# Kernel tuning notes

Hardware: AMD Instinct MI355X
Metric: run time of the kernel (lower is better)

## Reference

```python
import jax, jax.numpy as jnp
import numpy as np

B, S, D, H, DFF = 4, 1024, 1024, 16, 4096
DK = D // H
EPS = 1e-6


def setup_inputs() -> dict:
    key = jax.random.key(0)
    ks = jax.random.split(key, 16)
    sd = 0.02
    inp = {
        "x_v": jax.random.normal(ks[0], (B, S, D), jnp.float32),
        "x_k": jax.random.normal(ks[1], (B, S, D), jnp.float32),
        "x_q": jax.random.normal(ks[2], (B, S, D), jnp.float32),
        "mask": jnp.zeros((B, 1, S), jnp.float32),
        # per-head projections stacked: [H, D, DK]
        "wq": jax.random.normal(ks[3], (H, D, DK), jnp.float32) * sd,
        "bq": jnp.zeros((H, DK), jnp.float32),
        "wk": jax.random.normal(ks[4], (H, D, DK), jnp.float32) * sd,
        "bk": jnp.zeros((H, DK), jnp.float32),
        "wv": jax.random.normal(ks[5], (H, D, DK), jnp.float32) * sd,
        "bv": jnp.zeros((H, DK), jnp.float32),
        "w0": jax.random.normal(ks[6], (D, D), jnp.float32) * sd,
        "b0": jnp.zeros((D,), jnp.float32),
        "ln1_g": jnp.ones((D,), jnp.float32),
        "ln1_b": jnp.zeros((D,), jnp.float32),
        "ff1_w": jax.random.normal(ks[7], (D, DFF), jnp.float32) * sd,
        "ff1_b": jnp.zeros((DFF,), jnp.float32),
        "ff2_w": jax.random.normal(ks[8], (DFF, D), jnp.float32) * sd,
        "ff2_b": jnp.zeros((D,), jnp.float32),
        "ln2_g": jnp.ones((D,), jnp.float32),
        "ln2_b": jnp.zeros((D,), jnp.float32),
    }
    return inp


def layer_norm(x, g, b):
    mu = jnp.mean(x, axis=-1, keepdims=True)
    var = jnp.mean(jnp.square(x - mu), axis=-1, keepdims=True)
    return (x - mu) * jax.lax.rsqrt(var + EPS) * g + b


def reference(x_v, x_k, x_q, mask, wq, bq, wk, bk, wv, bv, w0, b0,
              ln1_g, ln1_b, ff1_w, ff1_b, ff2_w, ff2_b, ln2_g, ln2_b):
    # --- Multi-head attention (heads batched instead of Python loop) ---
    q = jnp.einsum('bsd,hdk->bhsk', x_q, wq) + bq[:, None, :]  # [B,H,S,DK]
    k = jnp.einsum('bsd,hdk->bhsk', x_k, wk) + bk[:, None, :]
    v = jnp.einsum('bsd,hdk->bhsk', x_v, wv) + bv[:, None, :]
    scores = jnp.einsum('bhqk,bhsk->bhqs', q, k) / jnp.sqrt(jnp.float32(DK))
    scores = scores + mask[:, None, :, :] * (-1e9)  # mask broadcast over heads
    attn_w = jax.nn.softmax(scores, axis=-1)        # [B,H,S,S]
    attn = jnp.einsum('bhqs,bhsk->bhqk', attn_w, v)  # [B,H,S,DK]
    concat = attn.transpose(0, 2, 1, 3).reshape(B, S, D)
    mha_out = concat @ w0 + b0
    # --- Residual + LayerNorm 1 (dropout is identity at inference) ---
    sub1 = layer_norm(x_q + mha_out, ln1_g, ln1_b)
    # --- Point-wise FFN ---
    ffn = jax.nn.relu(sub1 @ ff1_w + ff1_b) @ ff2_w + ff2_b
    # --- Residual + LayerNorm 2 ---
    out = layer_norm(sub1 + ffn, ln2_g, ln2_b)
    # original returns the attention weights of the LAST head only
    return out, attn_w[:, -1]
```

## Files before the change

kernel.cpp:

```cpp
#include <hip/hip_runtime.h>
#include <hip/hip_bf16.h>
#include <stdint.h>

#define DEV __device__ __forceinline__

typedef uint16_t u16;
typedef __attribute__((ext_vector_type(8))) short s16x8;
typedef __attribute__((ext_vector_type(8))) unsigned short u16x8;
typedef __attribute__((ext_vector_type(4))) unsigned short u16x4;
typedef __attribute__((ext_vector_type(4))) float f32x4;

constexpr int CB = 4;
constexpr int CS = 1024;
constexpr int CD = 1024;
constexpr int CH = 16;
constexpr int CDFF = 4096;
constexpr int LSTR = 72;

DEV float b2f(u16 u) { union { uint32_t i; float f; } v; v.i = (uint32_t)u << 16; return v.f; }
DEV u16 f2b(float f) {
  union { float f; uint32_t i; } v; v.f = f;
  uint32_t r = v.i + 0x7fffu + ((v.i >> 16) & 1u);
  return (u16)(r >> 16);
}

using as1v = const __attribute__((address_space(1))) void;
using as3v = __attribute__((address_space(3))) void;
DEV void g2l16(const u16* g, u16* l) {
  __builtin_amdgcn_global_load_lds((as1v*)g, (as3v*)l, 16, 0, 0);
}

__global__ void detect_dtype(const uint32_t* __restrict__ w, uint32_t* __restrict__ flag) {
  if (threadIdx.x == 0 && blockIdx.x == 0) {
    flag[0] = (w[0] == 0x3F800000u) ? 1u : 0u;
    flag[1] = 0u;
  }
}

__global__ __launch_bounds__(256)
void cvt3(const void* __restrict__ s0, const void* __restrict__ s1, const void* __restrict__ s2,
          u16* __restrict__ d0, u16* __restrict__ d1, u16* __restrict__ d2,
          const uint32_t* __restrict__ flag)
{
  const void* s = blockIdx.z == 0 ? s0 : (blockIdx.z == 1 ? s1 : s2);
  u16* d        = blockIdx.z == 0 ? d0 : (blockIdx.z == 1 ? d1 : d2);
  size_t i = ((size_t)blockIdx.x * 256 + threadIdx.x) * 4;
  if (flag[0]) {
    const float* f = (const float*)s;
    u16x4 o;
#pragma unroll
    for (int j = 0; j < 4; j++) o[j] = f2b(f[i + j]);
    *(u16x4*)(d + i) = o;
  } else {
    *(u16x4*)(d + i) = *(const u16x4*)((const u16*)s + i);
  }
}

struct SmallCvt {
  const void* src[11];
  u16* dst[11];
  int n[11];
};
__global__ __launch_bounds__(256)
void cvt_small(SmallCvt sc, const uint32_t* __restrict__ flag)
{
  int idx = blockIdx.x * 256 + threadIdx.x;
#pragma unroll
  for (int a = 0; a < 11; a++) {
    if (idx < sc.n[a]) {
      if (flag[0]) sc.dst[a][idx] = f2b(((const float*)sc.src[a])[idx]);
      else         sc.dst[a][idx] = ((const u16*)sc.src[a])[idx];
      return;
    }
    idx -= sc.n[a];
  }
}

__global__ __launch_bounds__(256)
void transpose64d(const void* __restrict__ in, u16* __restrict__ out,
                  int in_rs, long long in_ys, long long in_zs,
                  int out_rs, long long out_ys, long long out_zs,
                  const uint32_t* __restrict__ flag)
{
  int t = blockIdx.x * 256 + threadIdx.x;
  int k  = t & 63;
  int n8 = t >> 6;
  size_t ib = (size_t)blockIdx.z * in_zs + (size_t)blockIdx.y * in_ys
            + (size_t)n8 * 8 * in_rs + k;
  u16* ob = out + (size_t)blockIdx.z * out_zs + (size_t)blockIdx.y * out_ys
                + (size_t)k * out_rs + (size_t)n8 * 8;
  u16x8 v;
  if (flag[0]) {
    const float* f = (const float*)in;
#pragma unroll
    for (int j = 0; j < 8; j++) v[j] = f2b(f[ib + (size_t)j * in_rs]);
  } else {
    const u16* u = (const u16*)in;
#pragma unroll
    for (int j = 0; j < 8; j++) v[j] = u[ib + (size_t)j * in_rs];
  }
  *(u16x8*)ob = v;
}

struct GemmArgs {
  const u16* A[3];
  const u16* Bt[3];
  const u16* bias[3];
  u16* C[3];
  float scales[3];
  int M, N, K;
  int relu;
};

template<int MI, int NI, int WGM, int WGN>
DEV void gemm_body(const GemmArgs& g)
{
  constexpr int BM = WGM * MI * 16;
  constexpr int BN = WGN * NI * 16;
  constexpr int CHA = BM / 32;
  constexpr int CHB = BN / 32;

  const int z = blockIdx.z;
  const u16* __restrict__ A    = g.A[z];
  const u16* __restrict__ Bt   = g.Bt[z];
  const u16* __restrict__ bias = g.bias[z];
  u16* __restrict__ C          = g.C[z];
  const float scale = g.scales[z];
  const int N = g.N, K = g.K;

  __shared__ __align__(16) u16 lA[BM * 64];
  __shared__ __align__(16) u16 lB[BN * 64];

  const int tid  = threadIdx.x;
  const int lane = tid & 63;
  const int wave = tid >> 6;
  const int quad = lane >> 4;
  const int l16  = lane & 15;
  const int sw   = l16 & 7;
  const int wm = (wave / WGN) * MI * 16;
  const int wn = (wave % WGN) * NI * 16;

  const int flat = blockIdx.y * gridDim.x + blockIdx.x;
  const int nY = gridDim.y;
  const size_t bm = (size_t)(flat % nY) * BM;
  const size_t bn = (size_t)(flat / nY) * BN;

  f32x4 acc[MI][NI];
#pragma unroll
  for (int mi = 0; mi < MI; mi++)
#pragma unroll
    for (int ni = 0; ni < NI; ni++)
#pragma unroll
      for (int r = 0; r < 4; r++) acc[mi][ni][r] = 0.f;

  const u16* Ab = A + bm * K;
  const u16* Bb = Bt + bn * K;

  for (int k0 = 0; k0 < K; k0 += 64) {
#pragma unroll
    for (int i = 0; i < CHA; i++) {
      int c = i * 256 + tid;
      int r = c >> 3, j = c & 7;
      g2l16(Ab + (size_t)r * K + k0 + ((j ^ (r & 7)) * 8), lA + c * 8);
    }
#pragma unroll
    for (int i = 0; i < CHB; i++) {
      int c = i * 256 + tid;
      int r = c >> 3, j = c & 7;
      g2l16(Bb + (size_t)r * K + k0 + ((j ^ (r & 7)) * 8), lB + c * 8);
    }
    __syncthreads();
#pragma unroll
    for (int kk = 0; kk < 2; kk++) {
      s16x8 af[MI], bfr[NI];
#pragma unroll
      for (int mi = 0; mi < MI; mi++)
        af[mi] = *(const s16x8*)(lA + (wm + mi * 16 + l16) * 64 + (((kk * 4 + quad) ^ sw) * 8));
#pragma unroll
      for (int ni = 0; ni < NI; ni++)
        bfr[ni] = *(const s16x8*)(lB + (wn + ni * 16 + l16) * 64 + (((kk * 4 + quad) ^ sw) * 8));
#pragma unroll
      for (int mi = 0; mi < MI; mi++)
#pragma unroll
        for (int ni = 0; ni < NI; ni++)
          acc[mi][ni] = __builtin_amdgcn_mfma_f32_16x16x32_bf16(af[mi], bfr[ni], acc[mi][ni], 0, 0, 0);
    }
    __syncthreads();
  }

  float bvals[NI];
#pragma unroll
  for (int ni = 0; ni < NI; ni++) bvals[ni] = b2f(bias[bn + wn + ni * 16 + l16]);
#pragma unroll
  for (int mi = 0; mi < MI; mi++) {
#pragma unroll
    for (int r = 0; r < 4; r++) {
      size_t row = bm + wm + mi * 16 + quad * 4 + r;
      u16* crow = C + row * N + bn + wn;
#pragma unroll
      for (int ni = 0; ni < NI; ni++) {
        float v = (acc[mi][ni][r] + bvals[ni]) * scale;
        if (g.relu) v = fmaxf(v, 0.f);
        crow[ni * 16 + l16] = f2b(v);
      }
    }
  }
}

__global__ __launch_bounds__(256, 4) void gemm_qkv (GemmArgs g) { gemm_body<4, 4, 2, 2>(g); }
__global__ __launch_bounds__(256, 4) void gemm_wo  (GemmArgs g) { gemm_body<2, 2, 2, 2>(g); }
__global__ __launch_bounds__(256, 4) void gemm_ffn1(GemmArgs g) { gemm_body<4, 4, 2, 2>(g); }
__global__ __launch_bounds__(256, 4) void gemm_ffn2(GemmArgs g) { gemm_body<2, 2, 2, 2>(g); }

__global__ __launch_bounds__(256, 4)
void flash_attn(const u16* __restrict__ Qb, const u16* __restrict__ Kb,
                const u16* __restrict__ Vt, const u16* __restrict__ mask,
                u16* __restrict__ O, float* __restrict__ ml)
{
  const int b = blockIdx.z;
  const int h = blockIdx.x & 15;
  const int q0 = (blockIdx.x >> 4) * 64;
  const int tid  = threadIdx.x;
  const int lane = tid & 63, wave = tid >> 6;
  const int quad = lane >> 4, l16 = lane & 15;
  const int swz = l16 & 7;

  __shared__ __align__(16) u16 lK[64 * 64];
  __shared__ __align__(16) u16 lV[64 * 64];
  __shared__ __align__(16) u16 lP[4][16 * LSTR];

  s16x8 aq[2];
  {
    const u16* qp = Qb + ((size_t)b * CS + q0 + wave * 16 + l16) * CD + h * 64 + quad * 8;
    aq[0] = *(const s16x8*)qp;
    aq[1] = *(const s16x8*)(qp + 32);
  }

  f32x4 of[4];
  float m_r[4], l_r[4];
#pragma unroll
  for (int nt = 0; nt < 4; nt++)
#pragma unroll
    for (int r = 0; r < 4; r++) of[nt][r] = 0.f;
#pragma unroll
  for (int r = 0; r < 4; r++) { m_r[r] = -3.0e38f; l_r[r] = 0.f; }

  int srow[2], sj[2], wOff[2];
#pragma unroll
  for (int i = 0; i < 2; i++) {
    int c = i * 256 + tid;
    srow[i] = c >> 3;
    sj[i]   = c & 7;
    wOff[i] = srow[i] * 64 + ((sj[i] ^ (srow[i] & 7)) * 8);
  }

  const u16* Kbase = Kb + (size_t)b * CS * CD + h * 64;
  const u16* Vbase = Vt + ((size_t)(b * CH + h)) * 64 * CS;
  u16* lPw = lP[wave];

  u16x8 rk[2], rv[2];
#pragma unroll
  for (int i = 0; i < 2; i++) {
    rk[i] = *(const u16x8*)(Kbase + (size_t)srow[i] * CD + sj[i] * 8);
    rv[i] = *(const u16x8*)(Vbase + (size_t)srow[i] * CS + sj[i] * 8);
  }

  for (int kt = 0; kt < CS / 64; kt++) {
    __syncthreads();
#pragma unroll
    for (int i = 0; i < 2; i++) {
      *(u16x8*)(lK + wOff[i]) = rk[i];
      *(u16x8*)(lV + wOff[i]) = rv[i];
    }
    __syncthreads();

    if (kt + 1 < CS / 64) {
#pragma unroll
      for (int i = 0; i < 2; i++) {
        rk[i] = *(const u16x8*)(Kbase + (size_t)((kt + 1) * 64 + srow[i]) * CD + sj[i] * 8);
        rv[i] = *(const u16x8*)(Vbase + (size_t)srow[i] * CS + (kt + 1) * 64 + sj[i] * 8);
      }
    }

    f32x4 sf[4];
#pragma unroll
    for (int ni = 0; ni < 4; ni++)
#pragma unroll
      for (int r = 0; r < 4; r++) sf[ni][r] = 0.f;
#pragma unroll
    for (int kk = 0; kk < 2; kk++) {
#pragma unroll
      for (int ni = 0; ni < 4; ni++) {
        s16x8 bk = *(const s16x8*)(lK + (ni * 16 + l16) * 64 + (((kk * 4 + quad) ^ swz) * 8));
        sf[ni] = __builtin_amdgcn_mfma_f32_16x16x32_bf16(aq[kk], bk, sf[ni], 0, 0, 0);
      }
    }
#pragma unroll
    for (int ni = 0; ni < 4; ni++) {
      float mv = b2f(mask[(size_t)b * CS + kt * 64 + ni * 16 + l16]) * -1e9f;
#pragma unroll
      for (int r = 0; r < 4; r++) sf[ni][r] += mv;
    }
    float mx[4];
#pragma unroll
    for (int r = 0; r < 4; r++)
      mx[r] = fmaxf(fmaxf(sf[0][r], sf[1][r]), fmaxf(sf[2][r], sf[3][r]));
#pragma unroll
    for (int off = 1; off < 16; off <<= 1)
#pragma unroll
      for (int r = 0; r < 4; r++) mx[r] = fmaxf(mx[r], __shfl_xor(mx[r], off, 16));
    float al[4], ps[4];
#pragma unroll
    for (int r = 0; r < 4; r++) {
      float mn = fmaxf(m_r[r], mx[r]);
      al[r] = __expf(m_r[r] - mn);
      m_r[r] = mn;
      ps[r] = 0.f;
    }
#pragma unroll
    for (int ni = 0; ni < 4; ni++)
#pragma unroll
      for (int r = 0; r < 4; r++) {
        float p = __expf(sf[ni][r] - m_r[r]);
        sf[ni][r] = p;
        ps[r] += p;
      }
#pragma unroll
    for (int off = 1; off < 16; off <<= 1)
#pragma unroll
      for (int r = 0; r < 4; r++) ps[r] += __shfl_xor(ps[r], off, 16);
#pragma unroll
    for (int r = 0; r < 4; r++) l_r[r] = l_r[r] * al[r] + ps[r];
#pragma unroll
    for (int nt = 0; nt < 4; nt++)
#pragma unroll
      for (int r = 0; r < 4; r++) of[nt][r] *= al[r];
#pragma unroll
    for (int ni = 0; ni < 4; ni++)
#pragma unroll
      for (int r = 0; r < 4; r++)
        lPw[(quad * 4 + r) * LSTR + ni * 16 + l16] = f2b(sf[ni][r]);
#pragma unroll
    for (int kk = 0; kk < 2; kk++) {
      s16x8 ap = *(const s16x8*)(lPw + l16 * LSTR + kk * 32 + quad * 8);
#pragma unroll
      for (int nt = 0; nt < 4; nt++) {
        s16x8 bv = *(const s16x8*)(lV + (nt * 16 + l16) * 64 + (((kk * 4 + quad) ^ swz) * 8));
        of[nt] = __builtin_amdgcn_mfma_f32_16x16x32_bf16(ap, bv, of[nt], 0, 0, 0);
      }
    }
  }

#pragma unroll
  for (int r = 0; r < 4; r++) {
    float inv = 1.f / l_r[r];
    size_t row = q0 + wave * 16 + quad * 4 + r;
    u16* orow = O + ((size_t)b * CS + row) * CD + h * 64;
#pragma unroll
    for (int nt = 0; nt < 4; nt++) orow[nt * 16 + l16] = f2b(of[nt][r] * inv);
    if (h == CH - 1 && l16 == 0) {
      ml[(size_t)b * CS + row] = m_r[r];
      ml[(size_t)CB * CS + (size_t)b * CS + row] = l_r[r];
    }
  }
}

__global__ __launch_bounds__(256)
void attn_probs(const u16* __restrict__ Qb, const u16* __restrict__ Kb,
                const u16* __restrict__ mask, const float* __restrict__ ml,
                void* __restrict__ outbuf, const uint32_t* __restrict__ flag)
{
  const int b = blockIdx.z;
  const int h = CH - 1;
  const int q0 = blockIdx.x * 64;
  const int tid  = threadIdx.x;
  const int lane = tid & 63, wave = tid >> 6;
  const int quad = lane >> 4, l16 = lane & 15;
  const int swz = l16 & 7;
  const size_t OUT1 = (size_t)CB * CS * CD;
  const bool f32out = flag[0] != 0;

  __shared__ __align__(16) u16 lK[64 * 64];

  s16x8 aq[2];
  {
    const u16* qp = Qb + ((size_t)b * CS + q0 + wave * 16 + l16) * CD + h * 64 + quad * 8;
    aq[0] = *(const s16x8*)qp;
    aq[1] = *(const s16x8*)(qp + 32);
  }
  float mr[4], lr[4];
#pragma unroll
  for (int r = 0; r < 4; r++) {
    size_t row = q0 + wave * 16 + quad * 4 + r;
    mr[r] = ml[(size_t)b * CS + row];
    lr[r] = 1.f / ml[(size_t)CB * CS + (size_t)b * CS + row];
  }
  int srow[2], sj[2], wOff[2];
#pragma unroll
  for (int i = 0; i < 2; i++) {
    int c = i * 256 + tid;
    srow[i] = c >> 3;
    sj[i]   = c & 7;
    wOff[i] = srow[i] * 64 + ((sj[i] ^ (srow[i] & 7)) * 8);
  }
  const u16* Kbase = Kb + (size_t)b * CS * CD + h * 64;

  u16x8 rk[2];
#pragma unroll
  for (int i = 0; i < 2; i++)
    rk[i] = *(const u16x8*)(Kbase + (size_t)srow[i] * CD + sj[i] * 8);

  for (int kt = 0; kt < CS / 64; kt++) {
    __syncthreads();
#pragma unroll
    for (int i = 0; i < 2; i++)
      *(u16x8*)(lK + wOff[i]) = rk[i];
    __syncthreads();
    if (kt + 1 < CS / 64) {
#pragma unroll
      for (int i = 0; i < 2; i++)
        rk[i] = *(const u16x8*)(Kbase + (size_t)((kt + 1) * 64 + srow[i]) * CD + sj[i] * 8);
    }
    f32x4 sf[4];
#pragma unroll
    for (int ni = 0; ni < 4; ni++)
#pragma unroll
      for (int r = 0; r < 4; r++) sf[ni][r] = 0.f;
#pragma unroll
    for (int kk = 0; kk < 2; kk++) {
#pragma unroll
      for (int ni = 0; ni < 4; ni++) {
        s16x8 bk = *(const s16x8*)(lK + (ni * 16 + l16) * 64 + (((kk * 4 + quad) ^ swz) * 8));
        sf[ni] = __builtin_amdgcn_mfma_f32_16x16x32_bf16(aq[kk], bk, sf[ni], 0, 0, 0);
      }
    }
#pragma unroll
    for (int ni = 0; ni < 4; ni++) {
      float mv = b2f(mask[(size_t)b * CS + kt * 64 + ni * 16 + l16]) * -1e9f;
#pragma unroll
      for (int r = 0; r < 4; r++) {
        float p = __expf(sf[ni][r] + mv - mr[r]) * lr[r];
        size_t row = q0 + wave * 16 + quad * 4 + r;
        size_t idx = OUT1 + ((size_t)b * CS + row) * CS + kt * 64 + ni * 16 + l16;
        if (f32out) ((float*)outbuf)[idx] = p;
        else        ((u16*)outbuf)[idx] = f2b(p);
      }
    }
  }
}

__global__ __launch_bounds__(256)
void resid_ln(const u16* __restrict__ x, const u16* __restrict__ y,
              const u16* __restrict__ g, const u16* __restrict__ bb,
              void* __restrict__ out, const uint32_t* __restrict__ flag,
              int to_out)
{
  const int row = blockIdx.x;
  const int tid = threadIdx.x;
  __shared__ float rs[4], rs2[4];
  const u16* xr = x + (size_t)row * CD;
  const u16* yr = y + (size_t)row * CD;
  const int base = tid * 4;
  const bool f32out = to_out && (flag[0] != 0);
  float v[4];
  float s = 0.f, s2 = 0.f;
#pragma unroll
  for (int i = 0; i < 4; i++) {
    float a = b2f(xr[base + i]) + b2f(yr[base + i]);
    v[i] = a; s += a; s2 += a * a;
  }
#pragma unroll
  for (int off = 32; off > 0; off >>= 1) {
    s += __shfl_down(s, off, 64);
    s2 += __shfl_down(s2, off, 64);
  }
  if ((tid & 63) == 0) { rs[tid >> 6] = s; rs2[tid >> 6] = s2; }
  __syncthreads();
  float st = rs[0] + rs[1] + rs[2] + rs[3];
  float s2t = rs2[0] + rs2[1] + rs2[2] + rs2[3];
  float mu = st * (1.f / CD);
  float var = s2t * (1.f / CD) - mu * mu;
  float rstd = rsqrtf(var + 1e-6f);
#pragma unroll
  for (int i = 0; i < 4; i++) {
    float o = (v[i] - mu) * rstd * b2f(g[base + i]) + b2f(bb[base + i]);
    size_t idx = (size_t)row * CD + base + i;
    if (f32out) ((float*)out)[idx] = o;
    else        ((u16*)out)[idx] = f2b(o);
  }
}

extern "C" void kernel_launch(void* const* d_in, const int* in_sizes, int n_in,
                              void* d_out, int out_size, void* d_ws, size_t ws_size,
                              hipStream_t stream) {
  const void* x_v   = d_in[0];
  const void* x_k   = d_in[1];
  const void* x_q   = d_in[2];
  const void* maskI = d_in[3];
  const void* wq    = d_in[4];
  const void* bq    = d_in[5];
  const void* wk    = d_in[6];
  const void* bk    = d_in[7];
  const void* wv    = d_in[8];
  const void* bv    = d_in[9];
  const void* w0    = d_in[10];
  const void* b0    = d_in[11];
  const void* ln1_g = d_in[12];
  const void* ln1_b = d_in[13];
  const void* ff1_w = d_in[14];
  const void* ff1_b = d_in[15];
  const void* ff2_w = d_in[16];
  const void* ff2_b = d_in[17];
  const void* ln2_g = d_in[18];
  const void* ln2_b = d_in[19];

  u16* ws = (u16*)d_ws;
  size_t off = 0;
  auto alloc = [&](size_t n) { u16* p = ws + off; off += n; return p; };
  const size_t M1 = 1024 * 1024;
  u16* wqT   = alloc(M1);
  u16* wkT   = alloc(M1);
  u16* wvT   = alloc(M1);
  u16* w0T   = alloc(M1);
  u16* ff1T  = alloc(4 * M1);
  u16* ff2T  = alloc(4 * M1);
  u16* Qb    = alloc(4 * M1);
  u16* Kbuf  = alloc(4 * M1);
  u16* Vbuf  = alloc(4 * M1);
  u16* VtB   = alloc(4 * M1);
  u16* Ob    = alloc(4 * M1);
  u16* mha   = alloc(4 * M1);
  u16* sub1  = alloc(4 * M1);
  u16* ffmid = alloc(16 * M1);
  u16* cxq   = alloc(4 * M1);
  u16* cxk   = alloc(4 * M1);
  u16* cxv   = alloc(4 * M1);
  u16* cmask = alloc(4096);
  u16* cbq   = alloc(1024);
  u16* cbk   = alloc(1024);
  u16* cbv   = alloc(1024);
  u16* cb0   = alloc(1024);
  u16* cf1b  = alloc(4096);
  u16* cf2b  = alloc(1024);
  u16* cl1g  = alloc(1024);
  u16* cl1b  = alloc(1024);
  u16* cl2g  = alloc(1024);
  u16* cl2b  = alloc(1024);
  float* ml  = (float*)alloc(16384);
  uint32_t* flag = (uint32_t*)alloc(64);
  if (ws_size < off * sizeof(u16)) return;

  dim3 blk(256);

  detect_dtype<<<dim3(1), dim3(64), 0, stream>>>((const uint32_t*)ln1_g, flag);
  const uint32_t* fIn = flag;
  const uint32_t* fBf = flag + 1;

  cvt3<<<dim3(4096, 1, 3), blk, 0, stream>>>(x_q, x_k, x_v, cxq, cxk, cxv, fIn);
  {
    SmallCvt sc{};
    const void* s[11] = {maskI, bq, bk, bv, b0, ff1_b, ff2_b, ln1_g, ln1_b, ln2_g, ln2_b};
    u16* d[11] = {cmask, cbq, cbk, cbv, cb0, cf1b, cf2b, cl1g, cl1b, cl2g, cl2b};
    int n[11] = {4096, 1024, 1024, 1024, 1024, 4096, 1024, 1024, 1024, 1024, 1024};
    for (int i = 0; i < 11; i++) { sc.src[i] = s[i]; sc.dst[i] = d[i]; sc.n[i] = n[i]; }
    cvt_small<<<dim3(68), blk, 0, stream>>>(sc, fIn);
  }

  transpose64d<<<dim3(32, 16, 1), blk, 0, stream>>>(wq, wqT, 64, (long long)CD * 64, 0, CD, 64LL * CD, 0, fIn);
  transpose64d<<<dim3(32, 16, 1), blk, 0, stream>>>(wk, wkT, 64, (long long)CD * 64, 0, CD, 64LL * CD, 0, fIn);
  transpose64d<<<dim3(32, 16, 1), blk, 0, stream>>>(wv, wvT, 64, (long long)CD * 64, 0, CD, 64LL * CD, 0, fIn);
  transpose64d<<<dim3(32, 16, 1), blk, 0, stream>>>(w0, w0T, CD, 64, 0, CD, 64LL * CD, 0, fIn);
  transpose64d<<<dim3(32, 64, 1), blk, 0, stream>>>(ff1_w, ff1T, CDFF, 64, 0, CD, 64LL * CD, 0, fIn);
  transpose64d<<<dim3(128, 16, 1), blk, 0, stream>>>(ff2_w, ff2T, CD, 64, 0, CDFF, 64LL * CDFF, 0, fIn);

  {
    GemmArgs ga{};
    ga.A[0] = cxq;  ga.A[1] = cxk;  ga.A[2] = cxv;
    ga.Bt[0] = wqT; ga.Bt[1] = wkT; ga.Bt[2] = wvT;
    ga.bias[0] = cbq; ga.bias[1] = cbk; ga.bias[2] = cbv;
    ga.C[0] = Qb; ga.C[1] = Kbuf; ga.C[2] = Vbuf;
    ga.scales[0] = 0.125f; ga.scales[1] = 1.f; ga.scales[2] = 1.f;
    ga.M = CB * CS; ga.N = CD; ga.K = CD; ga.relu = 0;
    gemm_qkv<<<dim3(8, 32, 3), blk, 0, stream>>>(ga);
  }

  transpose64d<<<dim3(32, 16, 4), blk, 0, stream>>>(Vbuf, VtB, CD, 64, (long long)CS * CD,
                                                    CS, 64LL * CS, (long long)CH * 64 * CS, fBf);

  flash_attn<<<dim3(256, 1, CB), blk, 0, stream>>>(Qb, Kbuf, VtB, cmask, Ob, ml);

  attn_probs<<<dim3(CS / 64, 1, CB), blk, 0, stream>>>(Qb, Kbuf, cmask, ml, d_out, fIn);

  {
    GemmArgs ga{};
    ga.A[0] = Ob; ga.Bt[0] = w0T; ga.bias[0] = cb0; ga.C[0] = mha;
    ga.scales[0] = 1.f;
    ga.M = CB * CS; ga.N = CD; ga.K = CD; ga.relu = 0;
    gemm_wo<<<dim3(16, 64, 1), blk, 0, stream>>>(ga);
  }

  resid_ln<<<dim3(CB * CS), blk, 0, stream>>>(cxq, mha, cl1g, cl1b, sub1, fIn, 0);

  {
    GemmArgs ga{};
    ga.A[0] = sub1; ga.Bt[0] = ff1T; ga.bias[0] = cf1b; ga.C[0] = ffmid;
    ga.scales[0] = 1.f;
    ga.M = CB * CS; ga.N = CDFF; ga.K = CD; ga.relu = 1;
    gemm_ffn1<<<dim3(32, 32, 1), blk, 0, stream>>>(ga);
  }

  {
    GemmArgs ga{};
    ga.A[0] = ffmid; ga.Bt[0] = ff2T; ga.bias[0] = cf2b; ga.C[0] = mha;
    ga.scales[0] = 1.f;
    ga.M = CB * CS; ga.N = CD; ga.K = CDFF; ga.relu = 0;
    gemm_ffn2<<<dim3(16, 64, 1), blk, 0, stream>>>(ga);
  }

  resid_ln<<<dim3(CB * CS), blk, 0, stream>>>(sub1, mha, cl2g, cl2b, d_out, fIn, 1);
}
```

Before: 446.5 us.

## Use exp2 softmax with folded log2e, lazy rescale, packed bf16 cvt, taller out-proj tiles

Folds log2(e) into the Q scale and the mask constant so the flash attention and prob kernels can use exp2f in place of __expf. Skips the online-softmax rescale of the accumulator unless some row max in the wave grows by more than 8, which trades exact max tracking for bounded growth of the partial sums. P is converted to bf16 with the packed v_cvt_pk_bf16_f32 instruction. Separately, the Wo and FFN2 GEMMs use 4x2 warp tiles with half as many M blocks, for more reuse per block but fewer blocks in the grid.

```diff
diff --git a/kernel.cpp b/kernel.cpp
--- a/kernel.cpp
+++ b/kernel.cpp
@@ -16,6 +16,8 @@
 constexpr int CH = 16;
 constexpr int CDFF = 4096;
 constexpr int LSTR = 72;
+constexpr float QSCALE = 0.125f * 1.44269504f;
+constexpr float MASKC  = -1.44269504e9f;
 
 DEV float b2f(u16 u) { union { uint32_t i; float f; } v; v.i = (uint32_t)u << 16; return v.f; }
 DEV u16 f2b(float f) {
@@ -208,9 +210,9 @@
 }
 
 __global__ __launch_bounds__(256, 4) void gemm_qkv (GemmArgs g) { gemm_body<4, 4, 2, 2>(g); }
-__global__ __launch_bounds__(256, 4) void gemm_wo  (GemmArgs g) { gemm_body<2, 2, 2, 2>(g); }
+__global__ __launch_bounds__(256, 4) void gemm_wo  (GemmArgs g) { gemm_body<4, 2, 2, 2>(g); }
 __global__ __launch_bounds__(256, 4) void gemm_ffn1(GemmArgs g) { gemm_body<4, 4, 2, 2>(g); }
-__global__ __launch_bounds__(256, 4) void gemm_ffn2(GemmArgs g) { gemm_body<2, 2, 2, 2>(g); }
+__global__ __launch_bounds__(256, 4) void gemm_ffn2(GemmArgs g) { gemm_body<4, 2, 2, 2>(g); }
 
 __global__ __launch_bounds__(256, 4)
 void flash_attn(const u16* __restrict__ Qb, const u16* __restrict__ Kb,
@@ -297,7 +299,7 @@
     }
 #pragma unroll
     for (int ni = 0; ni < 4; ni++) {
-      float mv = b2f(mask[(size_t)b * CS + kt * 64 + ni * 16 + l16]) * -1e9f;
+      float mv = b2f(mask[(size_t)b * CS + kt * 64 + ni * 16 + l16]) * MASKC;
 #pragma unroll
       for (int r = 0; r < 4; r++) sf[ni][r] += mv;
     }
@@ -309,19 +311,25 @@
     for (int off = 1; off < 16; off <<= 1)
 #pragma unroll
       for (int r = 0; r < 4; r++) mx[r] = fmaxf(mx[r], __shfl_xor(mx[r], off, 16));
-    float al[4], ps[4];
-#pragma unroll
-    for (int r = 0; r < 4; r++) {
-      float mn = fmaxf(m_r[r], mx[r]);
-      al[r] = __expf(m_r[r] - mn);
-      m_r[r] = mn;
-      ps[r] = 0.f;
-    }
+    bool ng = (mx[0] <= m_r[0] + 8.f) && (mx[1] <= m_r[1] + 8.f) &&
+              (mx[2] <= m_r[2] + 8.f) && (mx[3] <= m_r[3] + 8.f);
+    if (!__all(ng)) {
+#pragma unroll
+      for (int r = 0; r < 4; r++) {
+        float mn = fmaxf(m_r[r], mx[r]);
+        float al = exp2f(m_r[r] - mn);
+        m_r[r] = mn;
+        l_r[r] *= al;
+#pragma unroll
+        for (int nt = 0; nt < 4; nt++) of[nt][r] *= al;
+      }
+    }
+    float ps[4] = {0.f, 0.f, 0.f, 0.f};
 #pragma unroll
     for (int ni = 0; ni < 4; ni++)
 #pragma unroll
       for (int r = 0; r < 4; r++) {
-        float p = __expf(sf[ni][r] - m_r[r]);
+        float p = exp2f(sf[ni][r] - m_r[r]);
         sf[ni][r] = p;
         ps[r] += p;
       }
@@ -330,16 +338,18 @@
 #pragma unroll
       for (int r = 0; r < 4; r++) ps[r] += __shfl_xor(ps[r], off, 16);
 #pragma unroll
-    for (int r = 0; r < 4; r++) l_r[r] = l_r[r] * al[r] + ps[r];
-#pragma unroll
-    for (int nt = 0; nt < 4; nt++)
-#pragma unroll
-      for (int r = 0; r < 4; r++) of[nt][r] *= al[r];
-#pragma unroll
-    for (int ni = 0; ni < 4; ni++)
-#pragma unroll
-      for (int r = 0; r < 4; r++)
-        lPw[(quad * 4 + r) * LSTR + ni * 16 + l16] = f2b(sf[ni][r]);
+    for (int r = 0; r < 4; r++) l_r[r] += ps[r];
+#pragma unroll
+    for (int ni = 0; ni < 4; ni++) {
+#pragma unroll
+      for (int j = 0; j < 2; j++) {
+        uint32_t pk;
+        asm("v_cvt_pk_bf16_f32 %0, %1, %2" : "=v"(pk)
+            : "v"(sf[ni][2 * j]), "v"(sf[ni][2 * j + 1]));
+        lPw[(quad * 4 + 2 * j) * LSTR + ni * 16 + l16] = (u16)pk;
+        lPw[(quad * 4 + 2 * j + 1) * LSTR + ni * 16 + l16] = (u16)(pk >> 16);
+      }
+    }
 #pragma unroll
     for (int kk = 0; kk < 2; kk++) {
       s16x8 ap = *(const s16x8*)(lPw + l16 * LSTR + kk * 32 + quad * 8);
@@ -436,10 +446,10 @@
     }
 #pragma unroll
     for (int ni = 0; ni < 4; ni++) {
-      float mv = b2f(mask[(size_t)b * CS + kt * 64 + ni * 16 + l16]) * -1e9f;
+      float mv = b2f(mask[(size_t)b * CS + kt * 64 + ni * 16 + l16]) * MASKC;
 #pragma unroll
       for (int r = 0; r < 4; r++) {
-        float p = __expf(sf[ni][r] + mv - mr[r]) * lr[r];
+        float p = exp2f(sf[ni][r] + mv - mr[r]) * lr[r];
         size_t row = q0 + wave * 16 + quad * 4 + r;
         size_t idx = OUT1 + ((size_t)b * CS + row) * CS + kt * 64 + ni * 16 + l16;
         if (f32out) ((float*)outbuf)[idx] = p;
@@ -579,7 +589,7 @@
     ga.Bt[0] = wqT; ga.Bt[1] = wkT; ga.Bt[2] = wvT;
     ga.bias[0] = cbq; ga.bias[1] = cbk; ga.bias[2] = cbv;
     ga.C[0] = Qb; ga.C[1] = Kbuf; ga.C[2] = Vbuf;
-    ga.scales[0] = 0.125f; ga.scales[1] = 1.f; ga.scales[2] = 1.f;
+    ga.scales[0] = QSCALE; ga.scales[1] = 1.f; ga.scales[2] = 1.f;
     ga.M = CB * CS; ga.N = CD; ga.K = CD; ga.relu = 0;
     gemm_qkv<<<dim3(8, 32, 3), blk, 0, stream>>>(ga);
   }
@@ -596,7 +606,7 @@
     ga.A[0] = Ob; ga.Bt[0] = w0T; ga.bias[0] = cb0; ga.C[0] = mha;
     ga.scales[0] = 1.f;
     ga.M = CB * CS; ga.N = CD; ga.K = CD; ga.relu = 0;
-    gemm_wo<<<dim3(16, 64, 1), blk, 0, stream>>>(ga);
+    gemm_wo<<<dim3(16, 32, 1), blk, 0, stream>>>(ga);
   }
 
   resid_ln<<<dim3(CB * CS), blk, 0, stream>>>(cxq, mha, cl1g, cl1b, sub1, fIn, 0);
@@ -614,7 +624,7 @@
     ga.A[0] = ffmid; ga.Bt[0] = ff2T; ga.bias[0] = cf2b; ga.C[0] = mha;
     ga.scales[0] = 1.f;
     ga.M = CB * CS; ga.N = CD; ga.K = CDFF; ga.relu = 0;
-    gemm_ffn2<<<dim3(16, 64, 1), blk, 0, stream>>>(ga);
+    gemm_ffn2<<<dim3(16, 32, 1), blk, 0, stream>>>(ga);
   }
 
   resid_ln<<<dim3(CB * CS), blk, 0, stream>>>(sub1, mha, cl2g, cl2b, d_out, fIn, 1);
```

New measurement: 461.3 us. 1.03x slower.
